# Kernel optimization log

Hardware: AMD Instinct MI355X
Metric: run time of the kernel (lower is better)

The kernel has to match this reference:

```python
import jax, jax.numpy as jnp
import numpy as np

# Standard minigrid color mapping (module references global COLOR_TO_IDX)
COLOR_TO_IDX = {'red': 0, 'green': 1, 'blue': 2, 'purple': 3, 'yellow': 4, 'grey': 5}
AGENT_FEATURE_SIZE = 13
NUM_AGENTS_PER_COLOR = {'grey': 4, 'yellow': 4}
COLOR_ORDER = sorted(NUM_AGENTS_PER_COLOR.keys())  # ['grey', 'yellow']
FEATURE_DIM = 256
B, N = 131072, 16
INPUT_DIM = (1 + sum(NUM_AGENTS_PER_COLOR.values())) * AGENT_FEATURE_SIZE  # 117


def setup_inputs() -> dict:
    key = jax.random.key(0)
    ks = jax.random.split(key, 14)
    inp = {
        'query_position': jax.random.normal(ks[0], (B, 2), jnp.float32),
        'query_direction': jax.random.normal(ks[1], (B, 4), jnp.float32),
        'query_abilities': jax.random.normal(ks[2], (B, 2), jnp.float32),
        'query_carried': jax.random.normal(ks[3], (B, 2), jnp.float32),
        'query_status': jax.random.normal(ks[4], (B, 3), jnp.float32),
        'all_agent_positions': jax.random.normal(ks[5], (B, N, 2), jnp.float32),
        'all_agent_directions': jax.random.normal(ks[6], (B, N, 4), jnp.float32),
        'all_agent_abilities': jax.random.normal(ks[7], (B, N, 2), jnp.float32),
        'all_agent_carried': jax.random.normal(ks[8], (B, N, 2), jnp.float32),
        'all_agent_status': jax.random.normal(ks[9], (B, N, 3), jnp.float32),
        'agent_color_indices': jax.random.randint(ks[10], (B, N), 0, 6, jnp.int32),
        # fc params; W stored (in, out) so y = x @ W + b (same math as torch Linear)
        'W': jax.random.normal(ks[11], (INPUT_DIM, FEATURE_DIM), jnp.float32) / np.sqrt(INPUT_DIM),
        'b': jax.random.normal(ks[12], (FEATURE_DIM,), jnp.float32) * 0.01,
    }
    return inp


def reference(query_position, query_direction, query_abilities, query_carried,
              query_status, all_agent_positions, all_agent_directions,
              all_agent_abilities, all_agent_carried, all_agent_status,
              agent_color_indices, W, b):
    batch = query_position.shape[0]
    # (B, N, 13) per-agent features, (B, 13) query features
    F = jnp.concatenate([all_agent_positions, all_agent_directions,
                         all_agent_abilities, all_agent_carried,
                         all_agent_status], axis=-1)
    query = jnp.concatenate([query_position, query_direction, query_abilities,
                             query_carried, query_status], axis=-1)
    feats = [query]
    rows = jnp.arange(batch)[:, None]  # (B, 1) for batched scatter
    for color in COLOR_ORDER:
        cidx = COLOR_TO_IDX[color]
        M = NUM_AGENTS_PER_COLOR[color]
        mask = agent_color_indices == cidx                 # (B, N)
        rank = jnp.cumsum(mask, axis=1) - 1                # slot of each matching agent
        valid = mask & (rank < M)
        slot = jnp.where(valid, rank, M)                   # dump overflow/non-match into slot M
        out = jnp.zeros((batch, M + 1, AGENT_FEATURE_SIZE), F.dtype)
        out = out.at[rows, slot].set(F)                    # unique (b, slot) per valid agent
        feats.append(out[:, :M].reshape(batch, M * AGENT_FEATURE_SIZE))
    x = jnp.concatenate(feats, axis=1)                     # (B, 117)
    return jax.nn.relu(x @ W + b)
```

## Files before the change

kernel.cpp:

```cpp
#include <hip/hip_runtime.h>


#define TM 128
#define XS_LD 136
#define THREADS 512
#define NCOL 256

typedef short short8 __attribute__((ext_vector_type(8)));
typedef float f32x4 __attribute__((ext_vector_type(4)));

__device__ __forceinline__ short f2bf(float x) {
    unsigned u = __builtin_bit_cast(unsigned, x);
    unsigned r = (u + 0x7fffu + ((u >> 16) & 1u)) >> 16;
    return (short)r;
}
__device__ __forceinline__ unsigned pk2(float a, float b) {
    return (unsigned)(unsigned short)f2bf(a) | ((unsigned)(unsigned short)f2bf(b) << 16);
}

__global__ __launch_bounds__(256)
void swz_w_kernel(const float* __restrict__ W, short* __restrict__ Wb) {
    const int idx  = blockIdx.x * 256 + threadIdx.x;
    const int j    = idx & 7;
    const int lane = (idx >> 3) & 63;
    const int ct   = (idx >> 9) & 3;
    const int kt   = (idx >> 11) & 3;
    const int cg   = (idx >> 13) & 3;
    const int kk   = kt * 32 + (lane >> 4) * 8 + j;
    const int u    = kk / 14;
    const int f    = kk - u * 14;
    const int col  = cg * 64 + ct * 16 + (lane & 15);
    float v = 0.f;
    if (u < 9 && f < 13) v = W[(u * 13 + f) * NCOL + col];
    Wb[idx] = f2bf(v);
}

template<bool WS>
__global__ __launch_bounds__(THREADS, 4)
void mga_encoder_kernel(const float* __restrict__ qpos, const float* __restrict__ qdir,
                        const float* __restrict__ qabil, const float* __restrict__ qcarr,
                        const float* __restrict__ qstat,
                        const float* __restrict__ apos, const float* __restrict__ adir,
                        const float* __restrict__ aabil, const float* __restrict__ acarr,
                        const float* __restrict__ astat,
                        const int* __restrict__ cidx,
                        const float* __restrict__ W, const float* __restrict__ bvec,
                        const short* __restrict__ Wb,
                        float* __restrict__ out) {
    __shared__ __align__(16) short Xs[TM * XS_LD];

    const int tid  = threadIdx.x;
    const int wave = tid >> 6;
    const int lane = tid & 63;
    const int ln   = lane & 15;
    const int q    = lane >> 4;
    const int r0w  = (wave & 1) * 64;
    const int cg   = wave >> 1;
    const int c0   = cg * 64;
    const int rowbase = blockIdx.x * TM;

    #pragma unroll
    for (int i = tid; i < TM * 5; i += THREADS) {
        const int row = i / 5, w = i - row * 5;
        *(unsigned*)&Xs[row * XS_LD + 126 + w * 2] = 0u;
    }

    const int rr  = tid >> 4;
    const int u   = tid & 15;
    const int grp = lane & 48;

    if (tid < TM) {
        const size_t b = (size_t)(rowbase + tid);
        const float2 qp = ((const float2*)qpos)[b];
        const float4 qd = ((const float4*)qdir)[b];
        const float2 qa = ((const float2*)qabil)[b];
        const float2 qc = ((const float2*)qcarr)[b];
        const float s0 = qstat[b * 3 + 0];
        const float s1 = qstat[b * 3 + 1];
        const float s2 = qstat[b * 3 + 2];
        unsigned* xd = (unsigned*)&Xs[tid * XS_LD];
        xd[0] = pk2(qp.x, qp.y); xd[1] = pk2(qd.x, qd.y);
        xd[2] = pk2(qd.z, qd.w); xd[3] = pk2(qa.x, qa.y);
        xd[4] = pk2(qc.x, qc.y); xd[5] = pk2(s0, s1);
        xd[6] = pk2(s2, 0.f);
    }

    int cs[4];
    #pragma unroll
    for (int p = 0; p < 4; p++)
        cs[p] = cidx[((size_t)(rowbase + p * 32 + rr)) * 16 + u];

    #pragma unroll
    for (int p = 0; p < 4; p++) {
        const int r = p * 32 + rr;
        const size_t b = (size_t)(rowbase + r);
        const size_t a = b * 16 + (size_t)u;

        const float2 pp = ((const float2*)apos)[a];
        const float4 dd = ((const float4*)adir)[a];
        const float2 ab = ((const float2*)aabil)[a];
        const float2 ca = ((const float2*)acarr)[a];
        const float s0 = astat[a * 3 + 0];
        const float s1 = astat[a * 3 + 1];
        const float s2 = astat[a * 3 + 2];
        unsigned d0 = pk2(pp.x, pp.y), d1 = pk2(dd.x, dd.y);
        unsigned d2 = pk2(dd.z, dd.w), d3 = pk2(ab.x, ab.y);
        unsigned d4 = pk2(ca.x, ca.y), d5 = pk2(s0, s1);
        unsigned d6 = pk2(s2, 0.f);

        const int c = cs[p];
        const unsigned long long bg = __ballot(c == 5);
        const unsigned long long by = __ballot(c == 4);

        int j = -1;
        if (u >= 1 && u <= 8) {
            unsigned mm = (unsigned)(((u <= 4) ? bg : by) >> grp) & 0xFFFFu;
            const int rank = (u - 1) & 3;
            mm = (rank > 0) ? (mm & (mm - 1)) : mm;
            mm = (rank > 1) ? (mm & (mm - 1)) : mm;
            mm = (rank > 2) ? (mm & (mm - 1)) : mm;
            j = mm ? (__ffs(mm) - 1) : -1;
        }
        const int src = grp + (j >= 0 ? j : u);

        unsigned e0 = (unsigned)__shfl((int)d0, src, 64);
        unsigned e1 = (unsigned)__shfl((int)d1, src, 64);
        unsigned e2 = (unsigned)__shfl((int)d2, src, 64);
        unsigned e3 = (unsigned)__shfl((int)d3, src, 64);
        unsigned e4 = (unsigned)__shfl((int)d4, src, 64);
        unsigned e5 = (unsigned)__shfl((int)d5, src, 64);
        unsigned e6 = (unsigned)__shfl((int)d6, src, 64);

        if (u >= 1 && u <= 8) {
            const bool ok = (j >= 0);
            unsigned* xd = (unsigned*)&Xs[r * XS_LD + 14 * u];
            xd[0] = ok ? e0 : 0u;  xd[1] = ok ? e1 : 0u;
            xd[2] = ok ? e2 : 0u;  xd[3] = ok ? e3 : 0u;
            xd[4] = ok ? e4 : 0u;  xd[5] = ok ? e5 : 0u;
            xd[6] = ok ? e6 : 0u;
        }
    }
    __syncthreads();

    const short8* Wf = (const short8*)Wb;
    #pragma unroll 1
    for (int h = 0; h < 2; h++) {
        short8 bfr[4][2];
        if constexpr (WS) {
            #pragma unroll
            for (int kt = 0; kt < 4; kt++)
                #pragma unroll
                for (int cc = 0; cc < 2; cc++)
                    bfr[kt][cc] = Wf[((cg * 4 + kt) * 4 + 2 * h + cc) * 64 + lane];
        } else {
            #pragma unroll
            for (int kt = 0; kt < 4; kt++)
                #pragma unroll
                for (int cc = 0; cc < 2; cc++) {
                    short8 fr;
                    #pragma unroll
                    for (int jj = 0; jj < 8; jj++) {
                        const int kk = kt * 32 + q * 8 + jj;
                        const int uu = kk / 14;
                        const int ff = kk - uu * 14;
                        float v = 0.f;
                        if (uu < 9 && ff < 13)
                            v = W[(uu * 13 + ff) * NCOL + c0 + (2 * h + cc) * 16 + ln];
                        fr[jj] = f2bf(v);
                    }
                    bfr[kt][cc] = fr;
                }
        }
        f32x4 bv[2];
        #pragma unroll
        for (int cc = 0; cc < 2; cc++)
            bv[cc] = *(const f32x4*)&bvec[c0 + (2 * h + cc) * 16 + q * 4];

        f32x4 acc[4][2];
        #pragma unroll
        for (int rt = 0; rt < 4; rt++)
            #pragma unroll
            for (int cc = 0; cc < 2; cc++) acc[rt][cc] = (f32x4){0.f, 0.f, 0.f, 0.f};

        #pragma unroll
        for (int kt = 0; kt < 4; kt++) {
            short8 av[4];
            #pragma unroll
            for (int rt = 0; rt < 4; rt++)
                av[rt] = *(const short8*)&Xs[(r0w + rt * 16 + ln) * XS_LD + kt * 32 + q * 8];
            #pragma unroll
            for (int rt = 0; rt < 4; rt++)
                #pragma unroll
                for (int cc = 0; cc < 2; cc++)
                    acc[rt][cc] = __builtin_amdgcn_mfma_f32_16x16x32_bf16(
                        bfr[kt][cc], av[rt], acc[rt][cc], 0, 0, 0);
        }

        #pragma unroll
        for (int rt = 0; rt < 4; rt++) {
            const int row = rowbase + r0w + rt * 16 + ln;
            #pragma unroll
            for (int cc = 0; cc < 2; cc++) {
                const int col = c0 + (2 * h + cc) * 16 + q * 4;
                f32x4 v;
                v[0] = fmaxf(acc[rt][cc][0] + bv[cc][0], 0.f);
                v[1] = fmaxf(acc[rt][cc][1] + bv[cc][1], 0.f);
                v[2] = fmaxf(acc[rt][cc][2] + bv[cc][2], 0.f);
                v[3] = fmaxf(acc[rt][cc][3] + bv[cc][3], 0.f);
                *(f32x4*)&out[(size_t)row * NCOL + col] = v;
            }
        }
    }
}

extern "C" void kernel_launch(void* const* d_in, const int* in_sizes, int n_in,
                              void* d_out, int out_size, void* d_ws, size_t ws_size,
                              hipStream_t stream) {
    const float* qpos  = (const float*)d_in[0];
    const float* qdir  = (const float*)d_in[1];
    const float* qabil = (const float*)d_in[2];
    const float* qcarr = (const float*)d_in[3];
    const float* qstat = (const float*)d_in[4];
    const float* apos  = (const float*)d_in[5];
    const float* adir  = (const float*)d_in[6];
    const float* aabil = (const float*)d_in[7];
    const float* acarr = (const float*)d_in[8];
    const float* astat = (const float*)d_in[9];
    const int*   cidx  = (const int*)d_in[10];
    const float* W     = (const float*)d_in[11];
    const float* bvec  = (const float*)d_in[12];
    float* out = (float*)d_out;

    const int B = in_sizes[0] / 2;
    const int nblocks = B / TM;

    const bool ws_ok = (d_ws != nullptr) && (ws_size >= 32768 * sizeof(short));
    if (ws_ok) {
        swz_w_kernel<<<128, 256, 0, stream>>>(W, (short*)d_ws);
        mga_encoder_kernel<true><<<nblocks, THREADS, 0, stream>>>(
            qpos, qdir, qabil, qcarr, qstat, apos, adir, aabil, acarr, astat,
            cidx, W, bvec, (const short*)d_ws, out);
    } else {
        mga_encoder_kernel<false><<<nblocks, THREADS, 0, stream>>>(
            qpos, qdir, qabil, qcarr, qstat, apos, adir, aabil, acarr, astat,
            cidx, W, bvec, nullptr, out);
    }
}
```

Before: 270.3 us.

## Make encoder persistent with register prefetch of next tile and double-buffered LDS

Launches a fixed grid of 256 blocks that loop over 128-row chunks instead of one block per chunk. Each iteration issues the global loads for the next chunk into registers before packing and running the MFMA GEMM on the current one, and LDS is double-buffered so the next chunk's staging does not overwrite data still being read. The aim is to hide global load latency behind compute and cut block launch overhead. In exchange, occupancy is lowered (launch bounds 4 to 2 blocks per SM) and register pressure rises from holding about 56 prefetched floats per thread. Only 256 blocks may underfill a 256-CU device if registers or LDS limit residency.

```diff
diff --git a/kernel.cpp b/kernel.cpp
--- a/kernel.cpp
+++ b/kernel.cpp
@@ -5,9 +5,12 @@
 #define XS_LD 136
 #define THREADS 512
 #define NCOL 256
+#define GRID 256
 
 typedef short short8 __attribute__((ext_vector_type(8)));
 typedef float f32x4 __attribute__((ext_vector_type(4)));
+
+struct Raw { float v[13]; };
 
 __device__ __forceinline__ short f2bf(float x) {
     unsigned u = __builtin_bit_cast(unsigned, x);
@@ -16,6 +19,38 @@
 }
 __device__ __forceinline__ unsigned pk2(float a, float b) {
     return (unsigned)(unsigned short)f2bf(a) | ((unsigned)(unsigned short)f2bf(b) << 16);
+}
+
+__device__ __forceinline__ void load_agent(const float* __restrict__ apos,
+                                           const float* __restrict__ adir,
+                                           const float* __restrict__ aabil,
+                                           const float* __restrict__ acarr,
+                                           const float* __restrict__ astat,
+                                           size_t a, Raw& r) {
+    const float2 pp = ((const float2*)apos)[a];
+    const float4 dd = ((const float4*)adir)[a];
+    const float2 ab = ((const float2*)aabil)[a];
+    const float2 ca = ((const float2*)acarr)[a];
+    r.v[0] = pp.x;  r.v[1] = pp.y;
+    r.v[2] = dd.x;  r.v[3] = dd.y;  r.v[4] = dd.z;  r.v[5] = dd.w;
+    r.v[6] = ab.x;  r.v[7] = ab.y;  r.v[8] = ca.x;  r.v[9] = ca.y;
+    r.v[10] = astat[a * 3 + 0]; r.v[11] = astat[a * 3 + 1]; r.v[12] = astat[a * 3 + 2];
+}
+
+__device__ __forceinline__ void load_query(const float* __restrict__ qpos,
+                                           const float* __restrict__ qdir,
+                                           const float* __restrict__ qabil,
+                                           const float* __restrict__ qcarr,
+                                           const float* __restrict__ qstat,
+                                           size_t b, Raw& r) {
+    const float2 qp = ((const float2*)qpos)[b];
+    const float4 qd = ((const float4*)qdir)[b];
+    const float2 qa = ((const float2*)qabil)[b];
+    const float2 qc = ((const float2*)qcarr)[b];
+    r.v[0] = qp.x;  r.v[1] = qp.y;
+    r.v[2] = qd.x;  r.v[3] = qd.y;  r.v[4] = qd.z;  r.v[5] = qd.w;
+    r.v[6] = qa.x;  r.v[7] = qa.y;  r.v[8] = qc.x;  r.v[9] = qc.y;
+    r.v[10] = qstat[b * 3 + 0]; r.v[11] = qstat[b * 3 + 1]; r.v[12] = qstat[b * 3 + 2];
 }
 
 __global__ __launch_bounds__(256)
@@ -36,7 +71,7 @@
 }
 
 template<bool WS>
-__global__ __launch_bounds__(THREADS, 4)
+__global__ __launch_bounds__(THREADS, 2)
 void mga_encoder_kernel(const float* __restrict__ qpos, const float* __restrict__ qdir,
                         const float* __restrict__ qabil, const float* __restrict__ qcarr,
                         const float* __restrict__ qstat,
@@ -46,8 +81,8 @@
                         const int* __restrict__ cidx,
                         const float* __restrict__ W, const float* __restrict__ bvec,
                         const short* __restrict__ Wb,
-                        float* __restrict__ out) {
-    __shared__ __align__(16) short Xs[TM * XS_LD];
+                        float* __restrict__ out, int nchunks) {
+    __shared__ __align__(16) short Xs[2][TM * XS_LD];
 
     const int tid  = threadIdx.x;
     const int wave = tid >> 6;
@@ -57,159 +92,190 @@
     const int r0w  = (wave & 1) * 64;
     const int cg   = wave >> 1;
     const int c0   = cg * 64;
-    const int rowbase = blockIdx.x * TM;
 
     #pragma unroll
-    for (int i = tid; i < TM * 5; i += THREADS) {
-        const int row = i / 5, w = i - row * 5;
-        *(unsigned*)&Xs[row * XS_LD + 126 + w * 2] = 0u;
-    }
+    for (int bz = 0; bz < 2; bz++)
+        for (int i = tid; i < TM * 5; i += THREADS) {
+            const int row = i / 5, w = i - row * 5;
+            *(unsigned*)&Xs[bz][row * XS_LD + 126 + w * 2] = 0u;
+        }
 
     const int rr  = tid >> 4;
     const int u   = tid & 15;
     const int grp = lane & 48;
-
-    if (tid < TM) {
-        const size_t b = (size_t)(rowbase + tid);
-        const float2 qp = ((const float2*)qpos)[b];
-        const float4 qd = ((const float4*)qdir)[b];
-        const float2 qa = ((const float2*)qabil)[b];
-        const float2 qc = ((const float2*)qcarr)[b];
-        const float s0 = qstat[b * 3 + 0];
-        const float s1 = qstat[b * 3 + 1];
-        const float s2 = qstat[b * 3 + 2];
-        unsigned* xd = (unsigned*)&Xs[tid * XS_LD];
-        xd[0] = pk2(qp.x, qp.y); xd[1] = pk2(qd.x, qd.y);
-        xd[2] = pk2(qd.z, qd.w); xd[3] = pk2(qa.x, qa.y);
-        xd[4] = pk2(qc.x, qc.y); xd[5] = pk2(s0, s1);
-        xd[6] = pk2(s2, 0.f);
+    const int grid = gridDim.x;
+
+    int tcur = blockIdx.x;
+    if (tcur >= nchunks) return;
+
+    Raw ar[4]; int cs[4]; Raw qr;
+    {
+        const int rowbase = tcur * TM;
+        #pragma unroll
+        for (int p = 0; p < 4; p++)
+            cs[p] = cidx[((size_t)(rowbase + p * 32 + rr)) * 16 + u];
+        #pragma unroll
+        for (int p = 0; p < 4; p++)
+            load_agent(apos, adir, aabil, acarr, astat,
+                       ((size_t)(rowbase + p * 32 + rr)) * 16 + (size_t)u, ar[p]);
+        if (tid < TM) load_query(qpos, qdir, qabil, qcarr, qstat,
+                                 (size_t)(rowbase + tid), qr);
     }
 
-    int cs[4];
-    #pragma unroll
-    for (int p = 0; p < 4; p++)
-        cs[p] = cidx[((size_t)(rowbase + p * 32 + rr)) * 16 + u];
-
-    #pragma unroll
-    for (int p = 0; p < 4; p++) {
-        const int r = p * 32 + rr;
-        const size_t b = (size_t)(rowbase + r);
-        const size_t a = b * 16 + (size_t)u;
-
-        const float2 pp = ((const float2*)apos)[a];
-        const float4 dd = ((const float4*)adir)[a];
-        const float2 ab = ((const float2*)aabil)[a];
-        const float2 ca = ((const float2*)acarr)[a];
-        const float s0 = astat[a * 3 + 0];
-        const float s1 = astat[a * 3 + 1];
-        const float s2 = astat[a * 3 + 2];
-        unsigned d0 = pk2(pp.x, pp.y), d1 = pk2(dd.x, dd.y);
-        unsigned d2 = pk2(dd.z, dd.w), d3 = pk2(ab.x, ab.y);
-        unsigned d4 = pk2(ca.x, ca.y), d5 = pk2(s0, s1);
-        unsigned d6 = pk2(s2, 0.f);
-
-        const int c = cs[p];
-        const unsigned long long bg = __ballot(c == 5);
-        const unsigned long long by = __ballot(c == 4);
-
-        int j = -1;
-        if (u >= 1 && u <= 8) {
-            unsigned mm = (unsigned)(((u <= 4) ? bg : by) >> grp) & 0xFFFFu;
-            const int rank = (u - 1) & 3;
-            mm = (rank > 0) ? (mm & (mm - 1)) : mm;
-            mm = (rank > 1) ? (mm & (mm - 1)) : mm;
-            mm = (rank > 2) ? (mm & (mm - 1)) : mm;
-            j = mm ? (__ffs(mm) - 1) : -1;
-        }
-        const int src = grp + (j >= 0 ? j : u);
-
-        unsigned e0 = (unsigned)__shfl((int)d0, src, 64);
-        unsigned e1 = (unsigned)__shfl((int)d1, src, 64);
-        unsigned e2 = (unsigned)__shfl((int)d2, src, 64);
-        unsigned e3 = (unsigned)__shfl((int)d3, src, 64);
-        unsigned e4 = (unsigned)__shfl((int)d4, src, 64);
-        unsigned e5 = (unsigned)__shfl((int)d5, src, 64);
-        unsigned e6 = (unsigned)__shfl((int)d6, src, 64);
-
-        if (u >= 1 && u <= 8) {
-            const bool ok = (j >= 0);
-            unsigned* xd = (unsigned*)&Xs[r * XS_LD + 14 * u];
-            xd[0] = ok ? e0 : 0u;  xd[1] = ok ? e1 : 0u;
-            xd[2] = ok ? e2 : 0u;  xd[3] = ok ? e3 : 0u;
-            xd[4] = ok ? e4 : 0u;  xd[5] = ok ? e5 : 0u;
-            xd[6] = ok ? e6 : 0u;
-        }
-    }
-    __syncthreads();
-
-    const short8* Wf = (const short8*)Wb;
-    #pragma unroll 1
-    for (int h = 0; h < 2; h++) {
-        short8 bfr[4][2];
-        if constexpr (WS) {
-            #pragma unroll
-            for (int kt = 0; kt < 4; kt++)
-                #pragma unroll
-                for (int cc = 0; cc < 2; cc++)
-                    bfr[kt][cc] = Wf[((cg * 4 + kt) * 4 + 2 * h + cc) * 64 + lane];
-        } else {
-            #pragma unroll
-            for (int kt = 0; kt < 4; kt++)
+    int buf = 0;
+    for (;;) {
+        const int tnext = tcur + grid;
+        const bool more = (tnext < nchunks);
+
+        Raw arn[4]; int csn[4]; Raw qrn;
+        if (more) {
+            const int rowbase = tnext * TM;
+            #pragma unroll
+            for (int p = 0; p < 4; p++)
+                csn[p] = cidx[((size_t)(rowbase + p * 32 + rr)) * 16 + u];
+            #pragma unroll
+            for (int p = 0; p < 4; p++)
+                load_agent(apos, adir, aabil, acarr, astat,
+                           ((size_t)(rowbase + p * 32 + rr)) * 16 + (size_t)u, arn[p]);
+            if (tid < TM) load_query(qpos, qdir, qabil, qcarr, qstat,
+                                     (size_t)(rowbase + tid), qrn);
+        }
+
+        if (tid < TM) {
+            unsigned* xd = (unsigned*)&Xs[buf][tid * XS_LD];
+            xd[0] = pk2(qr.v[0], qr.v[1]);   xd[1] = pk2(qr.v[2], qr.v[3]);
+            xd[2] = pk2(qr.v[4], qr.v[5]);   xd[3] = pk2(qr.v[6], qr.v[7]);
+            xd[4] = pk2(qr.v[8], qr.v[9]);   xd[5] = pk2(qr.v[10], qr.v[11]);
+            xd[6] = pk2(qr.v[12], 0.f);
+        }
+        #pragma unroll
+        for (int p = 0; p < 4; p++) {
+            const int r = p * 32 + rr;
+            const unsigned d0 = pk2(ar[p].v[0], ar[p].v[1]);
+            const unsigned d1 = pk2(ar[p].v[2], ar[p].v[3]);
+            const unsigned d2 = pk2(ar[p].v[4], ar[p].v[5]);
+            const unsigned d3 = pk2(ar[p].v[6], ar[p].v[7]);
+            const unsigned d4 = pk2(ar[p].v[8], ar[p].v[9]);
+            const unsigned d5 = pk2(ar[p].v[10], ar[p].v[11]);
+            const unsigned d6 = pk2(ar[p].v[12], 0.f);
+
+            const int c = cs[p];
+            const unsigned long long bg = __ballot(c == 5);
+            const unsigned long long by = __ballot(c == 4);
+
+            int j = -1;
+            if (u >= 1 && u <= 8) {
+                unsigned mm = (unsigned)(((u <= 4) ? bg : by) >> grp) & 0xFFFFu;
+                const int rank = (u - 1) & 3;
+                mm = (rank > 0) ? (mm & (mm - 1)) : mm;
+                mm = (rank > 1) ? (mm & (mm - 1)) : mm;
+                mm = (rank > 2) ? (mm & (mm - 1)) : mm;
+                j = mm ? (__ffs(mm) - 1) : -1;
+            }
+            const int src = grp + (j >= 0 ? j : u);
+
+            const unsigned e0 = (unsigned)__shfl((int)d0, src, 64);
+            const unsigned e1 = (unsigned)__shfl((int)d1, src, 64);
+            const unsigned e2 = (unsigned)__shfl((int)d2, src, 64);
+            const unsigned e3 = (unsigned)__shfl((int)d3, src, 64);
+            const unsigned e4 = (unsigned)__shfl((int)d4, src, 64);
+            const unsigned e5 = (unsigned)__shfl((int)d5, src, 64);
+            const unsigned e6 = (unsigned)__shfl((int)d6, src, 64);
+
+            if (u >= 1 && u <= 8) {
+                const bool ok = (j >= 0);
+                unsigned* xd = (unsigned*)&Xs[buf][r * XS_LD + 14 * u];
+                xd[0] = ok ? e0 : 0u;  xd[1] = ok ? e1 : 0u;
+                xd[2] = ok ? e2 : 0u;  xd[3] = ok ? e3 : 0u;
+                xd[4] = ok ? e4 : 0u;  xd[5] = ok ? e5 : 0u;
+                xd[6] = ok ? e6 : 0u;
+            }
+        }
+        __syncthreads();
+
+        const int rowbase = tcur * TM;
+        const short8* Wf = (const short8*)Wb;
+        #pragma unroll 1
+        for (int h = 0; h < 2; h++) {
+            short8 bfr[4][2];
+            if constexpr (WS) {
+                #pragma unroll
+                for (int kt = 0; kt < 4; kt++)
+                    #pragma unroll
+                    for (int cc = 0; cc < 2; cc++)
+                        bfr[kt][cc] = Wf[((cg * 4 + kt) * 4 + 2 * h + cc) * 64 + lane];
+            } else {
+                #pragma unroll
+                for (int kt = 0; kt < 4; kt++)
+                    #pragma unroll
+                    for (int cc = 0; cc < 2; cc++) {
+                        short8 fr;
+                        #pragma unroll
+                        for (int jj = 0; jj < 8; jj++) {
+                            const int kk = kt * 32 + q * 8 + jj;
+                            const int uu = kk / 14;
+                            const int ff = kk - uu * 14;
+                            float v = 0.f;
+                            if (uu < 9 && ff < 13)
+                                v = W[(uu * 13 + ff) * NCOL + c0 + (2 * h + cc) * 16 + ln];
+                            fr[jj] = f2bf(v);
+                        }
+                        bfr[kt][cc] = fr;
+                    }
+            }
+            f32x4 bv[2];
+            #pragma unroll
+            for (int cc = 0; cc < 2; cc++)
+                bv[cc] = *(const f32x4*)&bvec[c0 + (2 * h + cc) * 16 + q * 4];
+
+            f32x4 acc[4][2];
+            #pragma unroll
+            for (int rt = 0; rt < 4; rt++)
+                #pragma unroll
+                for (int cc = 0; cc < 2; cc++) acc[rt][cc] = (f32x4){0.f, 0.f, 0.f, 0.f};
+
+            #pragma unroll
+            for (int kt = 0; kt < 4; kt++) {
+                short8 av[4];
+                #pragma unroll
+                for (int rt = 0; rt < 4; rt++)
+                    av[rt] = *(const short8*)&Xs[buf][(r0w + rt * 16 + ln) * XS_LD + kt * 32 + q * 8];
+                #pragma unroll
+                for (int rt = 0; rt < 4; rt++)
+                    #pragma unroll
+                    for (int cc = 0; cc < 2; cc++)
+                        acc[rt][cc] = __builtin_amdgcn_mfma_f32_16x16x32_bf16(
+                            bfr[kt][cc], av[rt], acc[rt][cc], 0, 0, 0);
+            }
+
+            #pragma unroll
+            for (int rt = 0; rt < 4; rt++) {
+                const int row = rowbase + r0w + rt * 16 + ln;
                 #pragma unroll
                 for (int cc = 0; cc < 2; cc++) {
-                    short8 fr;
-                    #pragma unroll
-                    for (int jj = 0; jj < 8; jj++) {
-                        const int kk = kt * 32 + q * 8 + jj;
-                        const int uu = kk / 14;
-                        const int ff = kk - uu * 14;
-                        float v = 0.f;
-                        if (uu < 9 && ff < 13)
-                            v = W[(uu * 13 + ff) * NCOL + c0 + (2 * h + cc) * 16 + ln];
-                        fr[jj] = f2bf(v);
-                    }
-                    bfr[kt][cc] = fr;
+                    const int col = c0 + (2 * h + cc) * 16 + q * 4;
+                    f32x4 v;
+                    v[0] = fmaxf(acc[rt][cc][0] + bv[cc][0], 0.f);
+                    v[1] = fmaxf(acc[rt][cc][1] + bv[cc][1], 0.f);
+                    v[2] = fmaxf(acc[rt][cc][2] + bv[cc][2], 0.f);
+                    v[3] = fmaxf(acc[rt][cc][3] + bv[cc][3], 0.f);
+                    *(f32x4*)&out[(size_t)row * NCOL + col] = v;
                 }
-        }
-        f32x4 bv[2];
-        #pragma unroll
-        for (int cc = 0; cc < 2; cc++)
-            bv[cc] = *(const f32x4*)&bvec[c0 + (2 * h + cc) * 16 + q * 4];
-
-        f32x4 acc[4][2];
-        #pragma unroll
-        for (int rt = 0; rt < 4; rt++)
-            #pragma unroll
-            for (int cc = 0; cc < 2; cc++) acc[rt][cc] = (f32x4){0.f, 0.f, 0.f, 0.f};
-
-        #pragma unroll
-        for (int kt = 0; kt < 4; kt++) {
-            short8 av[4];
-            #pragma unroll
-            for (int rt = 0; rt < 4; rt++)
-                av[rt] = *(const short8*)&Xs[(r0w + rt * 16 + ln) * XS_LD + kt * 32 + q * 8];
-            #pragma unroll
-            for (int rt = 0; rt < 4; rt++)
-                #pragma unroll
-                for (int cc = 0; cc < 2; cc++)
-                    acc[rt][cc] = __builtin_amdgcn_mfma_f32_16x16x32_bf16(
-                        bfr[kt][cc], av[rt], acc[rt][cc], 0, 0, 0);
-        }
-
-        #pragma unroll
-        for (int rt = 0; rt < 4; rt++) {
-            const int row = rowbase + r0w + rt * 16 + ln;
-            #pragma unroll
-            for (int cc = 0; cc < 2; cc++) {
-                const int col = c0 + (2 * h + cc) * 16 + q * 4;
-                f32x4 v;
-                v[0] = fmaxf(acc[rt][cc][0] + bv[cc][0], 0.f);
-                v[1] = fmaxf(acc[rt][cc][1] + bv[cc][1], 0.f);
-                v[2] = fmaxf(acc[rt][cc][2] + bv[cc][2], 0.f);
-                v[3] = fmaxf(acc[rt][cc][3] + bv[cc][3], 0.f);
-                *(f32x4*)&out[(size_t)row * NCOL + col] = v;
-            }
-        }
+            }
+        }
+
+        if (!more) break;
+
+        #pragma unroll
+        for (int p = 0; p < 4; p++) {
+            cs[p] = csn[p];
+            #pragma unroll
+            for (int k = 0; k < 13; k++) ar[p].v[k] = arn[p].v[k];
+        }
+        #pragma unroll
+        for (int k = 0; k < 13; k++) qr.v[k] = qrn.v[k];
+        tcur = tnext;
+        buf ^= 1;
     }
 }
 
@@ -232,17 +298,18 @@
     float* out = (float*)d_out;
 
     const int B = in_sizes[0] / 2;
-    const int nblocks = B / TM;
+    const int nchunks = B / TM;
+    const int grid = nchunks < GRID ? nchunks : GRID;
 
     const bool ws_ok = (d_ws != nullptr) && (ws_size >= 32768 * sizeof(short));
     if (ws_ok) {
         swz_w_kernel<<<128, 256, 0, stream>>>(W, (short*)d_ws);
-        mga_encoder_kernel<true><<<nblocks, THREADS, 0, stream>>>(
+        mga_encoder_kernel<true><<<grid, THREADS, 0, stream>>>(
             qpos, qdir, qabil, qcarr, qstat, apos, adir, aabil, acarr, astat,
-            cidx, W, bvec, (const short*)d_ws, out);
+            cidx, W, bvec, (const short*)d_ws, out, nchunks);
     } else {
-        mga_encoder_kernel<false><<<nblocks, THREADS, 0, stream>>>(
+        mga_encoder_kernel<false><<<grid, THREADS, 0, stream>>>(
             qpos, qdir, qabil, qcarr, qstat, apos, adir, aabil, acarr, astat,
-            cidx, W, bvec, nullptr, out);
+            cidx, W, bvec, nullptr, out, nchunks);
     }
 }
```

Result: no change. 266.2 us (-1.5%).
